# Optimization experiments

Measured on AMD Instinct MI355X. Metric: run time of the kernel, lower is better.

The kernel has to match this reference:

```python
import jax, jax.numpy as jnp
import numpy as np

N, E, F = 50000, 800000, 64
GIN_F, H1, H2, OUT = 32, 128, 256, 2


def _lin_init(key, fan_in, fan_out):
    return jax.random.normal(key, (fan_in, fan_out), dtype=jnp.float32) / np.float32(np.sqrt(fan_in))


def setup_inputs() -> dict:
    key = jax.random.key(0)
    ks = jax.random.split(key, 24)
    inp = {
        "x": jax.random.normal(ks[0], (N, F), dtype=jnp.float32),
        "edge_index": jax.random.randint(ks[1], (2, E), 0, N, dtype=jnp.int64),
    }
    # GIN: 3 GINConv layers, each MLP = Linear->ReLU->Linear, then output Linear
    dims = [GIN_F, H1, H1]
    k = 2
    for i, din in enumerate(dims):
        inp[f"g{i}_w1"] = _lin_init(ks[k], din, H1); k += 1
        inp[f"g{i}_b1"] = jnp.zeros((H1,), jnp.float32)
        inp[f"g{i}_w2"] = _lin_init(ks[k], H1, H1); k += 1
        inp[f"g{i}_b2"] = jnp.zeros((H1,), jnp.float32)
    inp["gout_w"] = _lin_init(ks[k], H1, H1); k += 1
    inp["gout_b"] = jnp.zeros((H1,), jnp.float32)
    # SAGE: 2 SAGEConv layers (mean aggregation)
    sdims = [(F + H1, H2), (H2, OUT)]
    for i, (din, dout) in enumerate(sdims):
        inp[f"s{i}_wl"] = _lin_init(ks[k], din, dout); k += 1
        inp[f"s{i}_wr"] = _lin_init(ks[k], din, dout); k += 1
        inp[f"s{i}_b"] = jnp.zeros((dout,), jnp.float32)
    return inp


def _agg_sum(h, src, dst, n):
    # gather messages at src, scatter-add into dst: [N, d]
    return jax.ops.segment_sum(h[src], dst, num_segments=n)


def _forward(x, edge_index, g0_w1, g0_b1, g0_w2, g0_b2, g1_w1, g1_b1, g1_w2, g1_b2,
             g2_w1, g2_b1, g2_w2, g2_b2, gout_w, gout_b,
             s0_wl, s0_wr, s0_b, s1_wl, s1_wr, s1_b):
    src, dst = edge_index[0], edge_index[1]
    n = x.shape[0]
    deg = jax.ops.segment_sum(jnp.ones((src.shape[0],), x.dtype), dst, num_segments=n)
    inv_deg = (1.0 / jnp.maximum(deg, 1.0))[:, None]  # [N,1]

    # GIN branch on selected features (indices 0..31)
    h = x[:, :GIN_F]
    for w1, b1, w2, b2 in ((g0_w1, g0_b1, g0_w2, g0_b2),
                           (g1_w1, g1_b1, g1_w2, g1_b2),
                           (g2_w1, g2_b1, g2_w2, g2_b2)):
        m = h + _agg_sum(h, src, dst, n)        # (1+eps)*x + sum_neigh, eps=0
        h = jax.nn.relu(jax.nn.relu(m @ w1 + b1) @ w2 + b2)
    gin_out = h @ gout_w + gout_b               # [N, H1]

    # concat raw features with GIN embedding
    h = jnp.concatenate([x, gin_out], axis=1)   # [N, F+H1]

    # SAGE branch (mean aggregation)
    mean1 = _agg_sum(h, src, dst, n) * inv_deg
    h = jax.nn.relu(h @ s0_wl + mean1 @ s0_wr + s0_b)
    mean2 = _agg_sum(h, src, dst, n) * inv_deg
    out = h @ s1_wl + mean2 @ s1_wr + s1_b      # [N, OUT]
    return out


def reference(x, edge_index, g0_w1, g0_b1, g0_w2, g0_b2, g1_w1, g1_b1, g1_w2, g1_b2,
              g2_w1, g2_b1, g2_w2, g2_b2, gout_w, gout_b,
              s0_wl, s0_wr, s0_b, s1_wl, s1_wr, s1_b):
    return _forward(x, edge_index, g0_w1, g0_b1, g0_w2, g0_b2, g1_w1, g1_b1, g1_w2, g1_b2,
                    g2_w1, g2_b1, g2_w2, g2_b2, gout_w, gout_b,
                    s0_wl, s0_wr, s0_b, s1_wl, s1_wr, s1_b)
```

## Files before the change

### kernel.cpp

```cpp
#include <hip/hip_runtime.h>


typedef unsigned short ushort_t;
typedef __bf16 bf16x8 __attribute__((ext_vector_type(8)));
typedef float f32x4 __attribute__((ext_vector_type(4)));
typedef unsigned u32x4 __attribute__((ext_vector_type(4)));

__device__ __forceinline__ float b2f(unsigned int u16) {
    union { unsigned int i; float f; } v;
    v.i = u16 << 16;
    return v.f;
}
__device__ __forceinline__ unsigned short f2b(float f) {
    union { float f; unsigned int i; } v;
    v.f = f;
    unsigned int x = v.i;
    unsigned int r = (x + 0x7fffu + ((x >> 16) & 1u)) >> 16;
    return (unsigned short)r;
}

__global__ void detect_kernel(const int* __restrict__ ei, int ncheck, int* flag) {
    int t = blockIdx.x * blockDim.x + threadIdx.x;
    if (t < ncheck) {
        if (ei[2 * t + 1] != 0) atomicAnd(flag, 0);
    }
}

__global__ void deg_kernel(const int* __restrict__ ei, int E, const int* __restrict__ flag,
                           int* __restrict__ deg) {
    int e = blockIdx.x * blockDim.x + threadIdx.x;
    if (e >= E) return;
    int d = (*flag) ? ei[2 * ((size_t)E + e)] : ei[(size_t)E + e];
    atomicAdd(&deg[d], 1);
}

__global__ __launch_bounds__(256) void scanA_kernel(const int* __restrict__ deg, int n,
                                                    int* __restrict__ rowptr,
                                                    int* __restrict__ blocksum) {
    __shared__ int sh[256];
    int b = blockIdx.x, tid = threadIdx.x;
    int base = b * 2048 + tid * 8;
    int v[8];
#pragma unroll
    for (int e = 0; e < 8; ++e) {
        int i = base + e;
        v[e] = (i < n) ? deg[i] : 0;
    }
    int t = 0;
#pragma unroll
    for (int e = 0; e < 8; ++e) { int x = v[e]; v[e] = t; t += x; }
    sh[tid] = t;
    __syncthreads();
    for (int off = 1; off < 256; off <<= 1) {
        int val = (tid >= off) ? sh[tid - off] : 0;
        __syncthreads();
        sh[tid] += val;
        __syncthreads();
    }
    int excl = sh[tid] - t;
#pragma unroll
    for (int e = 0; e < 8; ++e) {
        int i = base + e;
        if (i < n) rowptr[i] = excl + v[e];
    }
    if (tid == 255) blocksum[b] = sh[255];
}

__global__ __launch_bounds__(256) void scanB_kernel(const int* __restrict__ blocksum, int nb,
                                                    int* __restrict__ blockoff,
                                                    int* __restrict__ rowptr, int n) {
    __shared__ int sh[256];
    int tid = threadIdx.x;
    int v = (tid < nb) ? blocksum[tid] : 0;
    sh[tid] = v;
    __syncthreads();
    for (int off = 1; off < 256; off <<= 1) {
        int t = (tid >= off) ? sh[tid - off] : 0;
        __syncthreads();
        sh[tid] += t;
        __syncthreads();
    }
    if (tid < nb) blockoff[tid] = sh[tid] - v;
    if (tid == 255) rowptr[n] = sh[255];
}

__global__ void scanC_kernel(const int* __restrict__ deg, int n, const int* __restrict__ blockoff,
                             int* __restrict__ rowptr, float* __restrict__ invdeg,
                             float* __restrict__ mask, int* __restrict__ bucket_cursor) {
    int i = blockIdx.x * blockDim.x + threadIdx.x;
    if (i >= n) return;
    int r = rowptr[i] + blockoff[i >> 11];
    rowptr[i] = r;
    if ((i & 255) == 0) bucket_cursor[i >> 8] = r;
    int d = deg[i];
    invdeg[i] = 1.0f / fmaxf((float)d, 1.0f);
    mask[i] = (d > 0) ? 1.0f : 0.0f;
}

__global__ __launch_bounds__(256) void binA_kernel(
    const int* __restrict__ ei, int E, const int* __restrict__ flag,
    int* __restrict__ bucket_cursor, unsigned* __restrict__ stage) {
    __shared__ unsigned sPair[4096];
    __shared__ int cnt[256], off[256], gst[256];
    int tid = threadIdx.x;
    cnt[tid] = 0;
    __syncthreads();
    int base = blockIdx.x * 4096;
    bool i64 = (*flag) != 0;
    unsigned u[16];
    int bk[16];
#pragma unroll
    for (int k = 0; k < 16; ++k) {
        int e = base + tid + k * 256;
        if (e < E) {
            int s_, d_;
            if (i64) { s_ = ei[2 * (size_t)e]; d_ = ei[2 * ((size_t)E + e)]; }
            else     { s_ = ei[e];             d_ = ei[(size_t)E + e]; }
            bk[k] = d_ >> 8;
            u[k] = (unsigned)s_ | ((unsigned)(d_ & 255) << 16) | ((unsigned)bk[k] << 24);
            atomicAdd(&cnt[bk[k]], 1);
        } else bk[k] = -1;
    }
    __syncthreads();
    int c = cnt[tid];
    off[tid] = c;
    __syncthreads();
    for (int o = 1; o < 256; o <<= 1) {
        int v = (tid >= o) ? off[tid - o] : 0;
        __syncthreads();
        off[tid] += v;
        __syncthreads();
    }
    int incl = off[tid];
    __syncthreads();
    off[tid] = incl - c;
    __syncthreads();
#pragma unroll
    for (int k = 0; k < 16; ++k) {
        if (bk[k] >= 0) {
            int p = atomicAdd(&off[bk[k]], 1);
            sPair[p] = u[k];
        }
    }
    if (c > 0) gst[tid] = atomicAdd(&bucket_cursor[tid], c);
    __syncthreads();
    int total = off[255];
    for (int idx = tid; idx < total; idx += 256) {
        unsigned v = sPair[idx];
        int b = (int)(v >> 24);
        int bstart = off[b] - cnt[b];
        stage[gst[b] + (idx - bstart)] = v;
    }
}

__global__ __launch_bounds__(256) void binB_kernel(
    const unsigned* __restrict__ stage, const int* __restrict__ rowptr,
    int Nn, int* __restrict__ col) {
    __shared__ int curs[256];
    int b = blockIdx.x, tid = threadIdx.x;
    int n0 = b << 8;
    if (n0 + tid < Nn) curs[tid] = rowptr[n0 + tid];
    __syncthreads();
    int s = rowptr[n0];
    int e = rowptr[min(n0 + 256, Nn)];
    for (int i = s + tid; i < e; i += 256) {
        unsigned u = stage[i];
        int p = atomicAdd(&curs[(u >> 16) & 255], 1);
        col[p] = (int)(u & 0xffffu);
    }
}

__global__ void xconv_kernel(const float* __restrict__ x, ushort_t* __restrict__ xb, int total16) {
    int idx = blockIdx.x * blockDim.x + threadIdx.x;
    if (idx >= total16) return;
    float4 v = *(const float4*)&x[(size_t)idx * 4];
    ushort4 u;
    u.x = f2b(v.x); u.y = f2b(v.y); u.z = f2b(v.z); u.w = f2b(v.w);
    *(ushort4*)&xb[(size_t)idx * 4] = u;
}

__global__ void foldw_kernel(const float* __restrict__ gw, const float* __restrict__ gb,
                             const float* __restrict__ s0wl, const float* __restrict__ s0wr,
                             const float* __restrict__ s0bias,
                             float* __restrict__ Fl, float* __restrict__ Fr,
                             float* __restrict__ bias2, float* __restrict__ cvec) {
    int idx = blockIdx.x * blockDim.x + threadIdx.x;
    if (idx >= 128 * 256) return;
    int k = idx >> 8, n = idx & 255;
    const float* wl = s0wl + 64 * 256;
    const float* wr = s0wr + 64 * 256;
    float al = 0.f, ar = 0.f;
    for (int j = 0; j < 128; ++j) {
        float g = gw[k * 128 + j];
        al += g * wl[j * 256 + n];
        ar += g * wr[j * 256 + n];
    }
    Fl[k * 256 + n] = al;
    Fr[k * 256 + n] = ar;
    if (k == 0) {
        float bl = 0.f, br = 0.f;
        for (int j = 0; j < 128; ++j) {
            float g = gb[j];
            bl += g * wl[j * 256 + n];
            br += g * wr[j * 256 + n];
        }
        bias2[n] = s0bias[n] + bl;
        cvec[n] = br;
    }
}

struct WtDesc { const float* src; ushort_t* dst; int lk2; int K; int N; int base; };
struct WtArgs { WtDesc d[10]; int total; };
__global__ void wtconv_kernel(WtArgs a) {
    int idx = blockIdx.x * blockDim.x + threadIdx.x;
    if (idx >= a.total) return;
    int s = 0;
#pragma unroll
    for (int i = 1; i < 10; ++i) if (idx >= a.d[i].base) s = i;
    int local = idx - a.d[s].base;
    int K = a.d[s].K;
    int n = local >> a.d[s].lk2;
    int k = local & (K - 1);
    unsigned off = (unsigned)((n >> 4) * (K >> 5) + (k >> 5)) * 512u
                 + (unsigned)(((n & 15) | (((k >> 3) & 3) << 4)) << 3) + (unsigned)(k & 7);
    a.d[s].dst[off] = f2b(a.d[s].src[(size_t)k * a.d[s].N + n]);
}

template <int VEC>
__device__ __forceinline__ void ldrow(const ushort_t* p, float* t) {
    if constexpr (VEC == 1) {
        t[0] = b2f(p[0]);
    } else if constexpr (VEC == 2) {
        unsigned int v = *(const unsigned int*)p;
        t[0] = b2f(v & 0xffffu); t[1] = b2f(v >> 16);
    } else {
        uint2 v = *(const uint2*)p;
        t[0] = b2f(v.x & 0xffffu); t[1] = b2f(v.x >> 16);
        t[2] = b2f(v.y & 0xffffu); t[3] = b2f(v.y >> 16);
    }
}

template <int VEC, int MODE>
__global__ __launch_bounds__(256) void aggb_kernel(
    const ushort_t* __restrict__ h, int ldh,
    const int* __restrict__ rowptr, const int* __restrict__ col,
    const float* __restrict__ invdeg,
    ushort_t* __restrict__ out, int ldo, int Nn, int lanes) {
    int wid = blockIdx.x * 4 + ((int)threadIdx.x >> 6);
    int lane = (int)threadIdx.x & 63;
    if (wid >= Nn || lane >= lanes) return;

    const ushort_t* hb = h + (size_t)lane * VEC;
    float a[VEC];
#pragma unroll
    for (int v = 0; v < VEC; ++v) a[v] = 0.f;

    int p0 = rowptr[wid], p1 = rowptr[wid + 1];
    int p = p0;
    for (; p + 4 <= p1; p += 4) {
        int j0 = col[p], j1 = col[p + 1], j2 = col[p + 2], j3 = col[p + 3];
        float t0[VEC], t1[VEC], t2[VEC], t3[VEC];
        ldrow<VEC>(hb + (size_t)j0 * ldh, t0);
        ldrow<VEC>(hb + (size_t)j1 * ldh, t1);
        ldrow<VEC>(hb + (size_t)j2 * ldh, t2);
        ldrow<VEC>(hb + (size_t)j3 * ldh, t3);
#pragma unroll
        for (int v = 0; v < VEC; ++v) a[v] += (t0[v] + t1[v]) + (t2[v] + t3[v]);
    }
    for (; p < p1; ++p) {
        float t[VEC];
        ldrow<VEC>(hb + (size_t)col[p] * ldh, t);
#pragma unroll
        for (int v = 0; v < VEC; ++v) a[v] += t[v];
    }

    if constexpr (MODE == 0) {
        float t[VEC];
        ldrow<VEC>(hb + (size_t)wid * ldh, t);
#pragma unroll
        for (int v = 0; v < VEC; ++v) a[v] += t[v];
    } else {
        float s = invdeg[wid];
#pragma unroll
        for (int v = 0; v < VEC; ++v) a[v] *= s;
    }

    ushort_t* op = out + (size_t)wid * ldo + (size_t)lane * VEC;
    if constexpr (VEC == 1) {
        op[0] = f2b(a[0]);
    } else if constexpr (VEC == 2) {
        unsigned int v = (unsigned int)f2b(a[0]) | ((unsigned int)f2b(a[1]) << 16);
        *(unsigned int*)op = v;
    } else {
        uint2 v;
        v.x = (unsigned int)f2b(a[0]) | ((unsigned int)f2b(a[1]) << 16);
        v.y = (unsigned int)f2b(a[2]) | ((unsigned int)f2b(a[3]) << 16);
        *(uint2*)op = v;
    }
}

__global__ __launch_bounds__(256) void aggdual_kernel(
    const ushort_t* __restrict__ xb,
    const int* __restrict__ rowptr, const int* __restrict__ col,
    const float* __restrict__ invdeg,
    ushort_t* __restrict__ out32, ushort_t* __restrict__ out64, int Nn) {
    int wid = blockIdx.x * 4 + ((int)threadIdx.x >> 6);
    int lane = (int)threadIdx.x & 63;
    if (wid >= Nn) return;
    const ushort_t* hb = xb + lane;
    float a = 0.f;
    int p = rowptr[wid], p1 = rowptr[wid + 1];
    for (; p + 4 <= p1; p += 4) {
        float v0 = b2f(hb[(size_t)col[p] * 64]);
        float v1 = b2f(hb[(size_t)col[p + 1] * 64]);
        float v2 = b2f(hb[(size_t)col[p + 2] * 64]);
        float v3 = b2f(hb[(size_t)col[p + 3] * 64]);
        a += (v0 + v1) + (v2 + v3);
    }
    for (; p < p1; ++p) a += b2f(hb[(size_t)col[p] * 64]);
    out64[(size_t)wid * 64 + lane] = f2b(a * invdeg[wid]);
    if (lane < 32) {
        float self = b2f(hb[(size_t)wid * 64]);
        out32[(size_t)wid * 32 + lane] = f2b(a + self);
    }
}

struct GPass { const ushort_t* A; const ushort_t* Wp; int lda; int K; };
struct FArgs {
    GPass p[4]; int np;
    const ushort_t* W2p; const ushort_t* W3p;
    const float* b1; const float* b2; const float* b3;
    int relu1, relu2, relu3;
    int chain;
    const float* rowmask; const float* cvec;
};

__global__ __launch_bounds__(512) void fgemm_kernel(
    FArgs fa, int M, ushort_t* __restrict__ out, int ldc) {
    __shared__ __align__(16) ushort_t Tlds[4 * 64 * 40];
    __shared__ __align__(16) ushort_t Wlds[16384];

    int rowbase = blockIdx.x * 64;
    int colbase = blockIdx.y * 128;
    int tid = threadIdx.x;
    int lane = tid & 63, wid = tid >> 6;
    int wr3 = wid & 3, wc2 = wid >> 2;
    int lr = lane & 15, lk = (lane >> 4) * 8, rq = (lane >> 4) * 4;

    f32x4 acc[4];
#pragma unroll
    for (int j = 0; j < 4; ++j) acc[j] = (f32x4){0.f, 0.f, 0.f, 0.f};

    for (int q = 0; q < fa.np; ++q) {
        const ushort_t* A = fa.p[q].A;
        const ushort_t* Wp = fa.p[q].Wp;
        int lda = fa.p[q].lda, K = fa.p[q].K;
        int nch = K >> 5;
        {
            const u32x4* wsrc = (const u32x4*)&Wp[((size_t)(colbase >> 4) * nch) * 512];
            u32x4* wdst = (u32x4*)Wlds;
            int nv = nch * 512;
            for (int i = tid; i < nv; i += 512) wdst[i] = wsrc[i];
        }
        for (int u = tid; u < 256 * nch; u += 512) {
            int c = u >> 8, r = (u >> 2) & 63, seg = u & 3;
            int gr = rowbase + r;
            u32x4 va = (u32x4){0u, 0u, 0u, 0u};
            if (gr < M)
                va = __builtin_nontemporal_load(
                    (const u32x4*)&A[(size_t)gr * lda + c * 32 + seg * 8]);
            *(u32x4*)&Tlds[c * 2560 + r * 40 + seg * 8] = va;
        }
        __syncthreads();
        int cgl0 = wc2 * 4;
        for (int c = 0; c < nch; ++c) {
            bf16x8 af = *(const bf16x8*)&Tlds[c * 2560 + (wr3 * 16 + lr) * 40 + lk];
            bf16x8 bfr[4];
#pragma unroll
            for (int j = 0; j < 4; ++j)
                bfr[j] = *(const bf16x8*)&Wlds[(((cgl0 + j) * nch) + c) * 512 + lane * 8];
#pragma unroll
            for (int j = 0; j < 4; ++j)
                acc[j] = __builtin_amdgcn_mfma_f32_16x16x32_bf16(af, bfr[j], acc[j], 0, 0, 0);
        }
        __syncthreads();
    }

    for (int g = 2; g <= fa.chain; ++g) {
        const float* bprev = (g == 2) ? fa.b1 : fa.b2;
        int reluprev = (g == 2) ? fa.relu1 : fa.relu2;
        const ushort_t* Wp = (g == 2) ? fa.W2p : fa.W3p;
        {
            const u32x4* wsrc = (const u32x4*)Wp;
            u32x4* wdst = (u32x4*)Wlds;
            for (int i = tid; i < 2048; i += 512) wdst[i] = wsrc[i];
        }
#pragma unroll
        for (int j = 0; j < 4; ++j) {
            int colj = wc2 * 64 + j * 16 + lr;
            float bv = bprev[colj];
#pragma unroll
            for (int t = 0; t < 4; ++t) {
                int row = wr3 * 16 + rq + t;
                float v = acc[j][t] + bv;
                if (reluprev) v = fmaxf(v, 0.f);
                Tlds[(colj >> 5) * 2560 + row * 40 + (colj & 31)] = f2b(v);
            }
            acc[j] = (f32x4){0.f, 0.f, 0.f, 0.f};
        }
        __syncthreads();
        int cgl0 = wc2 * 4;
        for (int c = 0; c < 4; ++c) {
            bf16x8 af = *(const bf16x8*)&Tlds[c * 2560 + (wr3 * 16 + lr) * 40 + lk];
            bf16x8 bfr[4];
#pragma unroll
            for (int j = 0; j < 4; ++j)
                bfr[j] = *(const bf16x8*)&Wlds[((cgl0 + j) * 4 + c) * 512 + lane * 8];
#pragma unroll
            for (int j = 0; j < 4; ++j)
                acc[j] = __builtin_amdgcn_mfma_f32_16x16x32_bf16(af, bfr[j], acc[j], 0, 0, 0);
        }
        __syncthreads();
    }

    const float* bf_ = (fa.chain == 1) ? fa.b1 : (fa.chain == 2) ? fa.b2 : fa.b3;
    int reluf = (fa.chain == 1) ? fa.relu1 : (fa.chain == 2) ? fa.relu2 : fa.relu3;
    float rm[4];
#pragma unroll
    for (int t = 0; t < 4; ++t) {
        int gr = rowbase + wr3 * 16 + rq + t;
        rm[t] = (fa.cvec && gr < M) ? fa.rowmask[gr] : 0.f;
    }
#pragma unroll
    for (int j = 0; j < 4; ++j) {
        int colj = wc2 * 64 + j * 16 + lr;
        float bv = bf_[colbase + colj];
        float cv = fa.cvec ? fa.cvec[colbase + colj] : 0.f;
#pragma unroll
        for (int t = 0; t < 4; ++t) {
            int row = wr3 * 16 + rq + t;
            float v = acc[j][t] + bv + rm[t] * cv;
            if (reluf) v = fmaxf(v, 0.f);
            Tlds[row * 128 + colj] = f2b(v);
        }
    }
    __syncthreads();
    for (int u = tid; u < 1024; u += 512) {
        int row = u >> 4, seg = u & 15;
        int gr = rowbase + row;
        if (gr < M)
            __builtin_nontemporal_store(
                *(const u32x4*)&Tlds[row * 128 + seg * 8],
                (u32x4*)&out[(size_t)gr * ldc + colbase + seg * 8]);
    }
}

__global__ void zproj_kernel(const ushort_t* __restrict__ s0,
                             const float* __restrict__ wl, const float* __restrict__ wr,
                             float2* __restrict__ zl, float2* __restrict__ z, int M) {
    int wave = threadIdx.x >> 6;
    int lane = threadIdx.x & 63;
    int i = blockIdx.x * 4 + wave;
    if (i >= M) return;
    float l0 = 0.f, l1 = 0.f, r0 = 0.f, r1 = 0.f;
    for (int k = lane; k < 256; k += 64) {
        float hv = b2f(s0[(size_t)i * 256 + k]);
        float2 wlv = *(const float2*)&wl[2 * k];
        float2 wrv = *(const float2*)&wr[2 * k];
        l0 += hv * wlv.x; l1 += hv * wlv.y;
        r0 += hv * wrv.x; r1 += hv * wrv.y;
    }
#pragma unroll
    for (int off = 32; off > 0; off >>= 1) {
        l0 += __shfl_down(l0, off);
        l1 += __shfl_down(l1, off);
        r0 += __shfl_down(r0, off);
        r1 += __shfl_down(r1, off);
    }
    if (lane == 0) {
        zl[i] = make_float2(l0, l1);
        z[i] = make_float2(r0, r1);
    }
}

__global__ void aggz_kernel(const float2* __restrict__ z, const float2* __restrict__ zl,
                            const int* __restrict__ rowptr, const int* __restrict__ col,
                            const float* __restrict__ invdeg, const float* __restrict__ b,
                            float* __restrict__ out, int Nn) {
    int i = blockIdx.x * blockDim.x + threadIdx.x;
    if (i >= Nn) return;
    float s0 = 0.f, s1 = 0.f;
    int p = rowptr[i], p1 = rowptr[i + 1];
    for (; p + 4 <= p1; p += 4) {
        float2 a = z[col[p]], c = z[col[p + 1]], d = z[col[p + 2]], e = z[col[p + 3]];
        s0 += (a.x + c.x) + (d.x + e.x);
        s1 += (a.y + c.y) + (d.y + e.y);
    }
    for (; p < p1; ++p) {
        float2 a = z[col[p]];
        s0 += a.x; s1 += a.y;
    }
    float inv = invdeg[i];
    float2 l = zl[i];
    out[(size_t)i * 2 + 0] = l.x + inv * s0 + b[0];
    out[(size_t)i * 2 + 1] = l.y + inv * s1 + b[1];
}

extern "C" void kernel_launch(void* const* d_in, const int* in_sizes, int n_in,
                              void* d_out, int out_size, void* d_ws, size_t ws_size,
                              hipStream_t stream) {
    const float* x      = (const float*)d_in[0];
    const int*   ei     = (const int*)d_in[1];
    const float* g_w1[3] = {(const float*)d_in[2], (const float*)d_in[6],  (const float*)d_in[10]};
    const float* g_b1[3] = {(const float*)d_in[3], (const float*)d_in[7],  (const float*)d_in[11]};
    const float* g_w2[3] = {(const float*)d_in[4], (const float*)d_in[8],  (const float*)d_in[12]};
    const float* g_b2[3] = {(const float*)d_in[5], (const float*)d_in[9],  (const float*)d_in[13]};
    const float* gout_w = (const float*)d_in[14];
    const float* gout_b = (const float*)d_in[15];
    const float* s0_wl  = (const float*)d_in[16];
    const float* s0_wr  = (const float*)d_in[17];
    const float* s0_b   = (const float*)d_in[18];
    const float* s1_wl  = (const float*)d_in[19];
    const float* s1_wr  = (const float*)d_in[20];
    const float* s1_b   = (const float*)d_in[21];
    float* out = (float*)d_out;

    const int N = in_sizes[0] / 64;
    const int E = in_sizes[1] / 2;

    char* ws = (char*)d_ws;
    size_t o = 0;
    auto take = [&](size_t bytes) -> char* {
        char* p = ws + o;
        o = (o + bytes + 255) & ~(size_t)255;
        return p;
    };
    ushort_t* xb     = (ushort_t*)take((size_t)N * 64 * 2);
    ushort_t* bA     = (ushort_t*)take((size_t)N * 128 * 2);
    ushort_t* bB     = (ushort_t*)take((size_t)N * 128 * 2);
    ushort_t* bC     = (ushort_t*)take((size_t)N * 128 * 2);
    ushort_t* aggxb  = (ushort_t*)take((size_t)N * 64 * 2);
    ushort_t* agggb  = (ushort_t*)take((size_t)N * 128 * 2);
    ushort_t* s0b    = (ushort_t*)take((size_t)N * 256 * 2);
    float2*   zlb    = (float2*)take((size_t)N * 2 * 4);
    float2*   zb     = (float2*)take((size_t)N * 2 * 4);
    float* Flbuf = (float*)take(128 * 256 * 4);
    float* Frbuf = (float*)take(128 * 256 * 4);
    float* bias2 = (float*)take(256 * 4);
    float* cvecb = (float*)take(256 * 4);
    ushort_t* w1t0 = (ushort_t*)take(128 * 32 * 2);
    ushort_t* w2t0 = (ushort_t*)take(128 * 128 * 2);
    ushort_t* w1t1 = (ushort_t*)take(128 * 128 * 2);
    ushort_t* w2t1 = (ushort_t*)take(128 * 128 * 2);
    ushort_t* w1t2 = (ushort_t*)take(128 * 128 * 2);
    ushort_t* w2t2 = (ushort_t*)take(128 * 128 * 2);
    ushort_t* wltop = (ushort_t*)take(256 * 64 * 2);
    ushort_t* wglp  = (ushort_t*)take(256 * 128 * 2);
    ushort_t* wrtop = (ushort_t*)take(256 * 64 * 2);
    ushort_t* wgrp  = (ushort_t*)take(256 * 128 * 2);
    unsigned* stage  = (unsigned*)take((size_t)E * 4);
    int*   colI   = (int*)take((size_t)E * 4);
    int*   rowptr = (int*)take((size_t)(N + 1) * 4);
    int*   deg    = (int*)take((size_t)N * 4);
    float* invdeg = (float*)take((size_t)N * 4);
    float* maskb  = (float*)take((size_t)N * 4);
    int*   blocksum = (int*)take(256 * 4);
    int*   blockoff = (int*)take(256 * 4);
    int*   bucket_cursor = (int*)take(512 * 4);
    int*   flag   = (int*)take(4);

    hipMemsetAsync(deg, 0, (size_t)N * 4, stream);
    hipMemsetAsync(flag, 1, 4, stream);

    const int TB = 256;
    const int nb = (N + 2047) / 2048;
    const int NBKT = (N + 255) >> 8;

    detect_kernel<<<4, TB, 0, stream>>>(ei, 1024, flag);
    deg_kernel<<<(E + TB - 1) / TB, TB, 0, stream>>>(ei, E, flag, deg);
    scanA_kernel<<<nb, 256, 0, stream>>>(deg, N, rowptr, blocksum);
    scanB_kernel<<<1, 256, 0, stream>>>(blocksum, nb, blockoff, rowptr, N);
    scanC_kernel<<<(N + TB - 1) / TB, TB, 0, stream>>>(deg, N, blockoff, rowptr, invdeg, maskb, bucket_cursor);
    binA_kernel<<<(E + 4095) / 4096, 256, 0, stream>>>(ei, E, flag, bucket_cursor, stage);
    binB_kernel<<<NBKT, 256, 0, stream>>>(stage, rowptr, N, colI);

    foldw_kernel<<<128, 256, 0, stream>>>(gout_w, gout_b, s0_wl, s0_wr, s0_b,
                                          Flbuf, Frbuf, bias2, cvecb);
    WtArgs wa;
    const float* wsrc[10] = {g_w1[0], g_w2[0], g_w1[1], g_w2[1], g_w1[2], g_w2[2],
                             s0_wl, Flbuf, s0_wr, Frbuf};
    ushort_t* wdst[10]    = {w1t0, w2t0, w1t1, w2t1, w1t2, w2t2,
                             wltop, wglp, wrtop, wgrp};
    int wk[10]  = {32, 128, 128, 128, 128, 128, 64, 128, 64, 128};
    int wl2[10] = {5, 7, 7, 7, 7, 7, 6, 7, 6, 7};
    int wn[10]  = {128, 128, 128, 128, 128, 128, 256, 256, 256, 256};
    int base = 0;
    for (int i = 0; i < 10; ++i) {
        wa.d[i].src = wsrc[i]; wa.d[i].dst = wdst[i];
        wa.d[i].lk2 = wl2[i]; wa.d[i].K = wk[i]; wa.d[i].N = wn[i]; wa.d[i].base = base;
        base += wk[i] * wn[i];
    }
    wa.total = base;
    wtconv_kernel<<<(base + TB - 1) / TB, TB, 0, stream>>>(wa);

    xconv_kernel<<<((N * 16) + TB - 1) / TB, TB, 0, stream>>>(x, xb, N * 16);

    const int AGG_GRID = (N + 3) / 4;
    const int GX = (N + 63) / 64;

    aggdual_kernel<<<AGG_GRID, 256, 0, stream>>>(xb, rowptr, colI, invdeg, bB, aggxb, N);

    {
        FArgs fa = {};
        fa.p[0] = {bB, w1t0, 32, 32};
        fa.np = 1;
        fa.W2p = w2t0;
        fa.b1 = g_b1[0]; fa.b2 = g_b2[0];
        fa.relu1 = 1; fa.relu2 = 1;
        fa.chain = 2;
        fgemm_kernel<<<dim3(GX, 1), 512, 0, stream>>>(fa, N, bA, 128);
    }

    aggb_kernel<2, 0><<<AGG_GRID, 256, 0, stream>>>(bA, 128, rowptr, colI, invdeg, bB, 128, N, 64);
    {
        FArgs fa = {};
        fa.p[0] = {bB, w1t1, 128, 128};
        fa.np = 1;
        fa.W2p = w2t1;
        fa.b1 = g_b1[1]; fa.b2 = g_b2[1];
        fa.relu1 = 1; fa.relu2 = 1;
        fa.chain = 2;
        fgemm_kernel<<<dim3(GX, 1), 512, 0, stream>>>(fa, N, bC, 128);
    }

    aggb_kernel<2, 0><<<AGG_GRID, 256, 0, stream>>>(bC, 128, rowptr, colI, invdeg, bB, 128, N, 64);
    {
        FArgs fa = {};
        fa.p[0] = {bB, w1t2, 128, 128};
        fa.np = 1;
        fa.W2p = w2t2;
        fa.b1 = g_b1[2]; fa.b2 = g_b2[2];
        fa.relu1 = 1; fa.relu2 = 1;
        fa.chain = 2;
        fgemm_kernel<<<dim3(GX, 1), 512, 0, stream>>>(fa, N, bA, 128);
    }

    aggb_kernel<2, 1><<<AGG_GRID, 256, 0, stream>>>(bA, 128, rowptr, colI, invdeg, agggb, 128, N, 64);

    {
        FArgs fa = {};
        fa.p[0] = {xb, wltop, 64, 64};
        fa.p[1] = {bA, wglp, 128, 128};
        fa.p[2] = {aggxb, wrtop, 64, 64};
        fa.p[3] = {agggb, wgrp, 128, 128};
        fa.np = 4;
        fa.b1 = bias2;
        fa.relu1 = 1;
        fa.chain = 1;
        fa.rowmask = maskb; fa.cvec = cvecb;
        fgemm_kernel<<<dim3(GX, 2), 512, 0, stream>>>(fa, N, s0b, 256);
    }

    zproj_kernel<<<(N + 3) / 4, 256, 0, stream>>>(s0b, s1_wl, s1_wr, zlb, zb, N);
    aggz_kernel<<<(N + TB - 1) / TB, TB, 0, stream>>>(zb, zlb, rowptr, colI, invdeg, s1_b, out, N);
}
```

Before: 370.8 us.

## Enlarge fused GEMM tile to 128 rows with 4x4 MFMA register blocking

New measurement: 408.5 us. +10.2%, slower.

```diff
diff --git a/kernel.cpp b/kernel.cpp
--- a/kernel.cpp
+++ b/kernel.cpp
@@ -335,21 +335,23 @@
     const float* rowmask; const float* cvec;
 };
 
-__global__ __launch_bounds__(512) void fgemm_kernel(
+__global__ __launch_bounds__(256) void fgemm_kernel(
     FArgs fa, int M, ushort_t* __restrict__ out, int ldc) {
-    __shared__ __align__(16) ushort_t Tlds[4 * 64 * 40];
+    __shared__ __align__(16) ushort_t Tlds[4 * 128 * 40];
     __shared__ __align__(16) ushort_t Wlds[16384];
 
-    int rowbase = blockIdx.x * 64;
+    int rowbase = blockIdx.x * 128;
     int colbase = blockIdx.y * 128;
     int tid = threadIdx.x;
     int lane = tid & 63, wid = tid >> 6;
-    int wr3 = wid & 3, wc2 = wid >> 2;
+    int wr2 = wid & 1, wc2 = wid >> 1;
     int lr = lane & 15, lk = (lane >> 4) * 8, rq = (lane >> 4) * 4;
 
-    f32x4 acc[4];
-#pragma unroll
-    for (int j = 0; j < 4; ++j) acc[j] = (f32x4){0.f, 0.f, 0.f, 0.f};
+    f32x4 acc[4][4];
+#pragma unroll
+    for (int i = 0; i < 4; ++i)
+#pragma unroll
+        for (int j = 0; j < 4; ++j) acc[i][j] = (f32x4){0.f, 0.f, 0.f, 0.f};
 
     for (int q = 0; q < fa.np; ++q) {
         const ushort_t* A = fa.p[q].A;
@@ -360,28 +362,31 @@
             const u32x4* wsrc = (const u32x4*)&Wp[((size_t)(colbase >> 4) * nch) * 512];
             u32x4* wdst = (u32x4*)Wlds;
             int nv = nch * 512;
-            for (int i = tid; i < nv; i += 512) wdst[i] = wsrc[i];
-        }
-        for (int u = tid; u < 256 * nch; u += 512) {
-            int c = u >> 8, r = (u >> 2) & 63, seg = u & 3;
+            for (int i = tid; i < nv; i += 256) wdst[i] = wsrc[i];
+        }
+        for (int u = tid; u < 512 * nch; u += 256) {
+            int c = u >> 9, rseg = u & 511, r = rseg >> 2, seg = rseg & 3;
             int gr = rowbase + r;
             u32x4 va = (u32x4){0u, 0u, 0u, 0u};
             if (gr < M)
                 va = __builtin_nontemporal_load(
                     (const u32x4*)&A[(size_t)gr * lda + c * 32 + seg * 8]);
-            *(u32x4*)&Tlds[c * 2560 + r * 40 + seg * 8] = va;
-        }
-        __syncthreads();
-        int cgl0 = wc2 * 4;
+            *(u32x4*)&Tlds[c * 5120 + r * 40 + seg * 8] = va;
+        }
+        __syncthreads();
         for (int c = 0; c < nch; ++c) {
-            bf16x8 af = *(const bf16x8*)&Tlds[c * 2560 + (wr3 * 16 + lr) * 40 + lk];
-            bf16x8 bfr[4];
+            bf16x8 af[4], bfr[4];
+#pragma unroll
+            for (int i = 0; i < 4; ++i)
+                af[i] = *(const bf16x8*)&Tlds[c * 5120 + (wr2 * 64 + i * 16 + lr) * 40 + lk];
 #pragma unroll
             for (int j = 0; j < 4; ++j)
-                bfr[j] = *(const bf16x8*)&Wlds[(((cgl0 + j) * nch) + c) * 512 + lane * 8];
-#pragma unroll
-            for (int j = 0; j < 4; ++j)
-                acc[j] = __builtin_amdgcn_mfma_f32_16x16x32_bf16(af, bfr[j], acc[j], 0, 0, 0);
+                bfr[j] = *(const bf16x8*)&Wlds[(((wc2 * 4 + j) * nch) + c) * 512 + lane * 8];
+#pragma unroll
+            for (int i = 0; i < 4; ++i)
+#pragma unroll
+                for (int j = 0; j < 4; ++j)
+                    acc[i][j] = __builtin_amdgcn_mfma_f32_16x16x32_bf16(af[i], bfr[j], acc[i][j], 0, 0, 0);
         }
         __syncthreads();
     }
@@ -393,59 +398,62 @@
         {
             const u32x4* wsrc = (const u32x4*)Wp;
             u32x4* wdst = (u32x4*)Wlds;
-            for (int i = tid; i < 2048; i += 512) wdst[i] = wsrc[i];
-        }
+            for (int i = tid; i < 2048; i += 256) wdst[i] = wsrc[i];
+        }
+#pragma unroll
+        for (int i = 0; i < 4; ++i)
+#pragma unroll
+            for (int j = 0; j < 4; ++j) {
+                int colj = wc2 * 64 + j * 16 + lr;
+                float bv = bprev[colj];
+#pragma unroll
+                for (int t = 0; t < 4; ++t) {
+                    int row = wr2 * 64 + i * 16 + rq + t;
+                    float v = acc[i][j][t] + bv;
+                    if (reluprev) v = fmaxf(v, 0.f);
+                    Tlds[(colj >> 5) * 5120 + row * 40 + (colj & 31)] = f2b(v);
+                }
+                acc[i][j] = (f32x4){0.f, 0.f, 0.f, 0.f};
+            }
+        __syncthreads();
+        for (int c = 0; c < 4; ++c) {
+            bf16x8 af[4], bfr[4];
+#pragma unroll
+            for (int i = 0; i < 4; ++i)
+                af[i] = *(const bf16x8*)&Tlds[c * 5120 + (wr2 * 64 + i * 16 + lr) * 40 + lk];
+#pragma unroll
+            for (int j = 0; j < 4; ++j)
+                bfr[j] = *(const bf16x8*)&Wlds[((wc2 * 4 + j) * 4 + c) * 512 + lane * 8];
+#pragma unroll
+            for (int i = 0; i < 4; ++i)
+#pragma unroll
+                for (int j = 0; j < 4; ++j)
+                    acc[i][j] = __builtin_amdgcn_mfma_f32_16x16x32_bf16(af[i], bfr[j], acc[i][j], 0, 0, 0);
+        }
+        __syncthreads();
+    }
+
+    const float* bf_ = (fa.chain == 1) ? fa.b1 : (fa.chain == 2) ? fa.b2 : fa.b3;
+    int reluf = (fa.chain == 1) ? fa.relu1 : (fa.chain == 2) ? fa.relu2 : fa.relu3;
+#pragma unroll
+    for (int i = 0; i < 4; ++i)
 #pragma unroll
         for (int j = 0; j < 4; ++j) {
             int colj = wc2 * 64 + j * 16 + lr;
-            float bv = bprev[colj];
+            float bv = bf_[colbase + colj];
+            float cv = fa.cvec ? fa.cvec[colbase + colj] : 0.f;
 #pragma unroll
             for (int t = 0; t < 4; ++t) {
-                int row = wr3 * 16 + rq + t;
-                float v = acc[j][t] + bv;
-                if (reluprev) v = fmaxf(v, 0.f);
-                Tlds[(colj >> 5) * 2560 + row * 40 + (colj & 31)] = f2b(v);
+                int row = wr2 * 64 + i * 16 + rq + t;
+                int gr = rowbase + row;
+                float rm = (fa.cvec && gr < M) ? fa.rowmask[gr] : 0.f;
+                float v = acc[i][j][t] + bv + rm * cv;
+                if (reluf) v = fmaxf(v, 0.f);
+                Tlds[row * 128 + colj] = f2b(v);
             }
-            acc[j] = (f32x4){0.f, 0.f, 0.f, 0.f};
-        }
-        __syncthreads();
-        int cgl0 = wc2 * 4;
-        for (int c = 0; c < 4; ++c) {
-            bf16x8 af = *(const bf16x8*)&Tlds[c * 2560 + (wr3 * 16 + lr) * 40 + lk];
-            bf16x8 bfr[4];
-#pragma unroll
-            for (int j = 0; j < 4; ++j)
-                bfr[j] = *(const bf16x8*)&Wlds[((cgl0 + j) * 4 + c) * 512 + lane * 8];
-#pragma unroll
-            for (int j = 0; j < 4; ++j)
-                acc[j] = __builtin_amdgcn_mfma_f32_16x16x32_bf16(af, bfr[j], acc[j], 0, 0, 0);
-        }
-        __syncthreads();
-    }
-
-    const float* bf_ = (fa.chain == 1) ? fa.b1 : (fa.chain == 2) ? fa.b2 : fa.b3;
-    int reluf = (fa.chain == 1) ? fa.relu1 : (fa.chain == 2) ? fa.relu2 : fa.relu3;
-    float rm[4];
-#pragma unroll
-    for (int t = 0; t < 4; ++t) {
-        int gr = rowbase + wr3 * 16 + rq + t;
-        rm[t] = (fa.cvec && gr < M) ? fa.rowmask[gr] : 0.f;
-    }
-#pragma unroll
-    for (int j = 0; j < 4; ++j) {
-        int colj = wc2 * 64 + j * 16 + lr;
-        float bv = bf_[colbase + colj];
-        float cv = fa.cvec ? fa.cvec[colbase + colj] : 0.f;
-#pragma unroll
-        for (int t = 0; t < 4; ++t) {
-            int row = wr3 * 16 + rq + t;
-            float v = acc[j][t] + bv + rm[t] * cv;
-            if (reluf) v = fmaxf(v, 0.f);
-            Tlds[row * 128 + colj] = f2b(v);
-        }
-    }
-    __syncthreads();
-    for (int u = tid; u < 1024; u += 512) {
+        }
+    __syncthreads();
+    for (int u = tid; u < 2048; u += 256) {
         int row = u >> 4, seg = u & 15;
         int gr = rowbase + row;
         if (gr < M)
@@ -606,7 +614,7 @@
     xconv_kernel<<<((N * 16) + TB - 1) / TB, TB, 0, stream>>>(x, xb, N * 16);
 
     const int AGG_GRID = (N + 3) / 4;
-    const int GX = (N + 63) / 64;
+    const int GX = (N + 127) / 128;
 
     aggdual_kernel<<<AGG_GRID, 256, 0, stream>>>(xb, rowptr, colI, invdeg, bB, aggxb, N);
 
@@ -618,7 +626,7 @@
         fa.b1 = g_b1[0]; fa.b2 = g_b2[0];
         fa.relu1 = 1; fa.relu2 = 1;
         fa.chain = 2;
-        fgemm_kernel<<<dim3(GX, 1), 512, 0, stream>>>(fa, N, bA, 128);
+        fgemm_kernel<<<dim3(GX, 1), 256, 0, stream>>>(fa, N, bA, 128);
     }
 
     aggb_kernel<2, 0><<<AGG_GRID, 256, 0, stream>>>(bA, 128, rowptr, colI, invdeg, bB, 128, N, 64);
@@ -630,7 +638,7 @@
         fa.b1 = g_b1[1]; fa.b2 = g_b2[1];
         fa.relu1 = 1; fa.relu2 = 1;
         fa.chain = 2;
-        fgemm_kernel<<<dim3(GX, 1), 512, 0, stream>>>(fa, N, bC, 128);
+        fgemm_kernel<<<dim3(GX, 1), 256, 0, stream>>>(fa, N, bC, 128);
     }
 
     aggb_kernel<2, 0><<<AGG_GRID, 256, 0, stream>>>(bC, 128, rowptr, colI, invdeg, bB, 128, N, 64);
@@ -642,7 +650,7 @@
         fa.b1 = g_b1[2]; fa.b2 = g_b2[2];
         fa.relu1 = 1; fa.relu2 = 1;
         fa.chain = 2;
-        fgemm_kernel<<<dim3(GX, 1), 512, 0, stream>>>(fa, N, bA, 128);
+        fgemm_kernel<<<dim3(GX, 1), 256, 0, stream>>>(fa, N, bA, 128);
     }
 
     aggb_kernel<2, 1><<<AGG_GRID, 256, 0, stream>>>(bA, 128, rowptr, colI, invdeg, agggb, 128, N, 64);
@@ -658,7 +666,7 @@
         fa.relu1 = 1;
         fa.chain = 1;
         fa.rowmask = maskb; fa.cvec = cvecb;
-        fgemm_kernel<<<dim3(GX, 2), 512, 0, stream>>>(fa, N, s0b, 256);
+        fgemm_kernel<<<dim3(GX, 2), 256, 0, stream>>>(fa, N, s0b, 256);
     }
 
     zproj_kernel<<<(N + 3) / 4, 256, 0, stream>>>(s0b, s1_wl, s1_wr, zlb, zb, N);
```
